# Optimization experiments

Measured on AMD Instinct MI355X. Metric: run time of the kernel, lower is better.

The kernel has to match this reference:

```python
import jax, jax.numpy as jnp
import numpy as np

B, T, C_IN, H, W = 64, 48, 64, 15, 15
HID, K, OUT = 128, 3, 128


def _conv(x, w, b):
    # x: [B, C, H, W], w: [4*HID, C, K, K] -> [B, 4*HID, H, W], SAME padding
    y = jax.lax.conv_general_dilated(
        x, w, window_strides=(1, 1), padding='SAME',
        dimension_numbers=('NCHW', 'OIHW', 'NCHW'))
    return y + b[None, :, None, None]


def _convlstm_layer(x_tm, w, b):
    # x_tm: time-major [T, B, C, H, W] -> hidden sequence [T, B, HID, H, W]
    h0 = jnp.zeros((x_tm.shape[1], HID, H, W), x_tm.dtype)
    c0 = jnp.zeros_like(h0)

    def step(carry, xt):
        h, c = carry
        z = _conv(jnp.concatenate([xt, h], axis=1), w, b)
        ig, fg, og, gg = jnp.split(z, 4, axis=1)
        i = jax.nn.sigmoid(ig)
        f = jax.nn.sigmoid(fg)
        o = jax.nn.sigmoid(og)
        g = jnp.tanh(gg)
        c_new = f * c + i * g
        h_new = o * jnp.tanh(c_new)
        return (h_new, c_new), h_new

    _, hs = jax.lax.scan(step, (h0, c0), x_tm)
    return hs


def setup_inputs() -> dict:
    key = jax.random.key(0)
    ks = jax.random.split(key, 7)
    s0 = 1.0 / np.sqrt((C_IN + HID) * K * K)
    s1 = 1.0 / np.sqrt((HID + HID) * K * K)
    sd = 1.0 / np.sqrt(HID * H * W)
    return {
        'encoder_output': jax.random.normal(ks[0], (B, T, C_IN, H, W), jnp.float32),
        'W0': jax.random.uniform(ks[1], (4 * HID, C_IN + HID, K, K), jnp.float32, -s0, s0),
        'b0': jax.random.uniform(ks[2], (4 * HID,), jnp.float32, -s0, s0),
        'W1': jax.random.uniform(ks[3], (4 * HID, HID + HID, K, K), jnp.float32, -s1, s1),
        'b1': jax.random.uniform(ks[4], (4 * HID,), jnp.float32, -s1, s1),
        'Wd': jax.random.uniform(ks[5], (HID * H * W, OUT), jnp.float32, -sd, sd),
        'bd': jax.random.uniform(ks[6], (OUT,), jnp.float32, -sd, sd),
    }


def reference(encoder_output, W0, b0, W1, b1, Wd, bd):
    x_tm = jnp.swapaxes(encoder_output, 0, 1)  # [T, B, C, H, W]
    h1 = _convlstm_layer(x_tm, W0, b0)          # [T, B, HID, H, W]
    h2 = _convlstm_layer(h1, W1, b1)            # [T, B, HID, H, W]
    last = h2[-1]                               # [B, HID, H, W] (last timestep)
    feat = last.reshape(last.shape[0], -1)      # dropout is identity in eval
    return feat @ Wd + bd
```

## Files before the change

kernel.cpp:

```cpp
#include <hip/hip_runtime.h>
#include <stdint.h>


typedef unsigned int u32;
typedef unsigned short u16;
typedef __attribute__((ext_vector_type(8))) short short8;
typedef __attribute__((ext_vector_type(4))) float f32x4;

#define NB    64
#define NT    48
#define NCX   64
#define NHID  128
#define NPIX  225
#define MTOT  (NB*NPIX)
#define MT_TILES 113
#define RROWS 18544
#define AROWS 224
#define L1BLK 216
#define L2BLK 288

__device__ __forceinline__ u32 bf16_rne(u32 u) {
  return (u + 0x7fffu + ((u >> 16) & 1u)) >> 16;
}
__device__ __forceinline__ float bf2f(u16 h) { return __uint_as_float(((u32)h) << 16); }
__device__ __forceinline__ void split2(float f, u32& hi, u32& lo) {
  u32 u = __float_as_uint(f);
  hi = bf16_rne(u);
  lo = bf16_rne(__float_as_uint(f - __uint_as_float(hi << 16)));
}
__device__ __forceinline__ void splitpair(u32 p0, u32 p1, u32& hw, u32& lw) {
  u32 s0, s1; u32 h0, l0, h1, l1;
  split2(__uint_as_float(p0), h0, l0);
  split2(__uint_as_float(p1), h1, l1);
  hw = (h1 << 16) | h0; lw = (l1 << 16) | l0;
  (void)s0; (void)s1;
}
__device__ __forceinline__ float sigmoidf_(float x) { return 1.f / (1.f + __expf(-x)); }
__device__ __forceinline__ float tanhf_(float x) {
  float e = __expf(-2.f * fabsf(x));
  return copysignf((1.f - e) / (1.f + e), x);
}
__device__ __forceinline__ void gl_lds16(const void* g, void* l) {
  __builtin_amdgcn_global_load_lds(
      (const __attribute__((address_space(1))) u32*)(g),
      (__attribute__((address_space(3))) u32*)(l), 16, 0, 0);
}

__global__ void prep_kernel(const float* __restrict__ W0, const float* __restrict__ b0,
                            const float* __restrict__ W1, const float* __restrict__ b1,
                            u16* __restrict__ Wi, float* __restrict__ bp) {
  const int total = (L1BLK + L2BLK) * 8192 + 1024;
  for (int idx = blockIdx.x * blockDim.x + threadIdx.x; idx < total;
       idx += gridDim.x * blockDim.x) {
    if (idx < (L1BLK + L2BLK) * 8192) {
      const int blk = idx >> 13, o = idx & 8191;
      int nt, cg, tap, CINL;
      const float* W;
      if (blk < L1BLK) { nt = blk / 54; cg = (blk % 54) / 9; tap = blk % 9; CINL = 192; W = W0; }
      else { const int b2 = blk - L1BLK; nt = b2 / 72; cg = (b2 % 72) / 9; tap = b2 % 9; CINL = 256; W = W1; }
      const int pl = o >> 12, kg = (o >> 10) & 3, qrow = (o >> 3) & 127, j = o & 7;
      const int q = nt * 128 + qrow;
      const int hid = ((q >> 6) << 4) | (q & 15), gate = (q >> 4) & 3;
      const int co = gate * 128 + hid;
      const int ci = cg * 32 + kg * 8 + j;
      const float wv = W[(size_t)co * (CINL * 9) + ci * 9 + tap];
      u32 hi, lo; split2(wv, hi, lo);
      Wi[idx] = (u16)(pl ? lo : hi);
    } else {
      const int e2 = idx - (L1BLK + L2BLK) * 8192;
      const int l = e2 >> 9, q = e2 & 511;
      const int hid = ((q >> 6) << 4) | (q & 15), gate = (q >> 4) & 3;
      bp[e2] = (l == 0 ? b0 : b1)[gate * 128 + hid];
    }
  }
}

template <int LAYER>
__device__ __forceinline__ void step_body(
    uint4* ldsA, uint4* ldsB, int mt, int nt,
    const float* __restrict__ x, int t,
    const u16* __restrict__ P1h, const u16* __restrict__ P1l,
    const u16* __restrict__ P2h, const u16* __restrict__ P2l,
    u16* __restrict__ Wh, u16* __restrict__ Wl,
    const u16* __restrict__ Wimg, const float* __restrict__ bp,
    float* __restrict__ c)
{
  constexpr int CG = (LAYER == 1) ? 6 : 8;
  const int tid = threadIdx.x, lane = tid & 63, w = tid >> 6;
  const int wave_m = (w >> 1) * 64, wave_n = (w & 1) * 64;
  const int kgc = lane >> 4, l15 = lane & 15;

  const int m0 = mt * 128;
  const int b0v = m0 / 225, p0v = m0 - b0v * 225;
  const int r0 = b0v * 289 + (p0v / 15) * 17 + (p0v % 15);

  int aoff[4];
  #pragma unroll
  for (int mb = 0; mb < 4; ++mb) {
    int m = m0 + wave_m + mb * 16 + l15; if (m > 14399) m = 14399;
    const int b = m / 225, p = m - b * 225;
    const int r = b * 289 + (p / 15) * 17 + (p % 15) + 18;
    aoff[mb] = (kgc * AROWS + (r - r0 - 18)) * 16;
  }
  int boff[4];
  #pragma unroll
  for (int nb = 0; nb < 4; ++nb) boff[nb] = (kgc * 128 + wave_n + l15 + nb * 16) * 16;

  f32x4 acc[4][4];
  #pragma unroll
  for (int i = 0; i < 4; ++i)
    #pragma unroll
    for (int j = 0; j < 4; ++j) acc[i][j] = (f32x4){0.f, 0.f, 0.f, 0.f};

  auto stageA_h = [&](const u16* __restrict__ Ph, const u16* __restrict__ Pl, int choff) {
    #pragma unroll
    for (int i = 0; i < 7; ++i) {
      const int chunk = w * 7 + i;
      const int e = chunk * 64 + lane;
      const int pk = e / AROWS, row = e - pk * AROWS;
      const int kg = pk & 3;
      const u16* P = (pk >= 4) ? Pl : Ph;
      const char* src = (const char*)P + ((size_t)(r0 + row) * 128 + choff + kg * 8) * 2;
      gl_lds16(src, (char*)ldsA + chunk * 1024);
    }
  };
  auto stageA_x = [&](int cg) {
    for (int tau = tid; tau < 4 * AROWS; tau += 256) {
      const int kg = tau / AROWS, row = tau - kg * AROWS;
      const int rg = r0 + row;
      const int rb = rg / 289, rr = rg - rb * 289;
      const int rh = rr / 17 - 1, rw = rr - (rr / 17) * 17 - 1;
      const bool v = ((unsigned)rh < 15u) && ((unsigned)rw < 15u) && (rb < 64);
      const int p = rh * 15 + rw;
      const float* src = x + (((size_t)rb * NT + t) * NCX + cg * 32 + kg * 8) * NPIX + p;
      u32 hw_[4], lw_[4];
      #pragma unroll
      for (int jj = 0; jj < 4; ++jj) {
        const float f0 = v ? src[(2 * jj) * NPIX] : 0.f;
        const float f1 = v ? src[(2 * jj + 1) * NPIX] : 0.f;
        u32 h0, l0, h1, l1;
        split2(f0, h0, l0); split2(f1, h1, l1);
        hw_[jj] = (h1 << 16) | h0; lw_[jj] = (l1 << 16) | l0;
      }
      ldsA[kg * AROWS + row]       = make_uint4(hw_[0], hw_[1], hw_[2], hw_[3]);
      ldsA[(4 + kg) * AROWS + row] = make_uint4(lw_[0], lw_[1], lw_[2], lw_[3]);
    }
  };
  auto stageB = [&](int cg, int tap, int bufsel) {
    const char* src = (const char*)Wimg + ((size_t)((nt * CG + cg) * 9 + tap) << 14);
    char* dstb = (char*)(ldsB + bufsel * 1024);
    #pragma unroll
    for (int j = 0; j < 4; ++j) {
      const int chunk = w * 4 + j;
      gl_lds16(src + chunk * 1024 + lane * 16, dstb + chunk * 1024);
    }
  };

  int bufsel = 0;
  for (int cg = 0; cg < CG; ++cg) {
    if (LAYER == 1 && cg < 2) stageA_x(cg);
    else if (LAYER == 1)      stageA_h(P1h, P1l, (cg - 2) * 32);
    else if (cg < 4)          stageA_h(P1h, P1l, cg * 32);
    else                      stageA_h(P2h, P2l, (cg - 4) * 32);
    if (cg == 0) stageB(0, 0, bufsel);
    __syncthreads();

    #pragma unroll
    for (int tap = 0; tap < 9; ++tap) {
      if (tap < 8)            stageB(cg, tap + 1, bufsel ^ 1);
      else if (cg + 1 < CG)   stageB(cg + 1, 0, bufsel ^ 1);
      {
        const int DPO = ((tap / 3) * 17 + (tap % 3)) * 16;
        const char* A  = (const char*)ldsA;
        const char* Bb = (const char*)(ldsB + bufsel * 1024);
        short8 ah[4], al[4], bh[4], bl[4];
        #pragma unroll
        for (int mb = 0; mb < 4; ++mb) {
          ah[mb] = *(const short8*)(A + aoff[mb] + DPO);
          al[mb] = *(const short8*)(A + aoff[mb] + DPO + 14336);
        }
        #pragma unroll
        for (int nb = 0; nb < 4; ++nb) {
          bh[nb] = *(const short8*)(Bb + boff[nb]);
          bl[nb] = *(const short8*)(Bb + boff[nb] + 8192);
        }
        __builtin_amdgcn_s_setprio(1);
        #pragma unroll
        for (int mb = 0; mb < 4; ++mb)
          #pragma unroll
          for (int nb = 0; nb < 4; ++nb) {
            acc[mb][nb] = __builtin_amdgcn_mfma_f32_16x16x32_bf16(ah[mb], bh[nb], acc[mb][nb], 0, 0, 0);
            acc[mb][nb] = __builtin_amdgcn_mfma_f32_16x16x32_bf16(al[mb], bh[nb], acc[mb][nb], 0, 0, 0);
            acc[mb][nb] = __builtin_amdgcn_mfma_f32_16x16x32_bf16(ah[mb], bl[nb], acc[mb][nb], 0, 0, 0);
          }
        __builtin_amdgcn_s_setprio(0);
      }
      __syncthreads();
      bufsel ^= 1;
    }
  }

  const int colq = nt * 128 + wave_n;
  const int hid  = ((colq >> 6) << 4) + l15;
  const float bi  = bp[colq +      l15];
  const float bf_ = bp[colq + 16 + l15];
  const float bo  = bp[colq + 32 + l15];
  const float bg  = bp[colq + 48 + l15];
  #pragma unroll
  for (int mb = 0; mb < 4; ++mb) {
    #pragma unroll
    for (int rr = 0; rr < 4; ++rr) {
      const int m = m0 + wave_m + mb * 16 + ((lane >> 4) << 2) + rr;
      if (m < MTOT) {
        const float gi = sigmoidf_(acc[mb][0][rr] + bi);
        const float gf = sigmoidf_(acc[mb][1][rr] + bf_);
        const float go = sigmoidf_(acc[mb][2][rr] + bo);
        const float gg = tanhf_   (acc[mb][3][rr] + bg);
        const size_t cidx = (size_t)m * NHID + hid;
        const float cn = gf * c[cidx] + gi * gg;
        c[cidx] = cn;
        const float h = go * tanhf_(cn);
        u32 hh, hl2; split2(h, hh, hl2);
        const int b = m / 225, p = m - b * 225;
        const size_t r = (size_t)b * 289 + (p / 15) * 17 + (p % 15) + 18;
        Wh[r * 128 + hid] = (u16)hh;
        Wl[r * 128 + hid] = (u16)hl2;
      }
    }
  }
}

__global__ __launch_bounds__(256, 2)
void steps_kernel(const float* __restrict__ x, int t1,
                  const u16* __restrict__ h1hr, const u16* __restrict__ h1lr,
                  const u16* __restrict__ h2hr, const u16* __restrict__ h2lr,
                  u16* __restrict__ h1hw, u16* __restrict__ h1lw,
                  u16* __restrict__ h2hw, u16* __restrict__ h2lw,
                  const u16* __restrict__ Wi, const float* __restrict__ bp,
                  float* __restrict__ c1, float* __restrict__ c2, int do_l2) {
  __shared__ uint4 ldsA[1792];
  __shared__ uint4 ldsB[2048];
  int bid = ((int)blockIdx.z * 4 + (int)blockIdx.y) * MT_TILES + (int)blockIdx.x;
  int nid = bid;
  if (gridDim.z == 2) nid = (bid & 7) * MT_TILES + (bid >> 3);
  const int z   = nid / (MT_TILES * 4);
  const int rem = nid - z * (MT_TILES * 4);
  const int nt  = rem / MT_TILES;
  const int mt  = rem - nt * MT_TILES;
  if (z == 0 && do_l2)
    step_body<2>(ldsA, ldsB, mt, nt, nullptr, 0, h1hr, h1lr, h2hr, h2lr,
                 h2hw, h2lw, Wi + (size_t)L1BLK * 8192, bp + 512, c2);
  else
    step_body<1>(ldsA, ldsB, mt, nt, x, t1, h1hr, h1lr, nullptr, nullptr,
                 h1hw, h1lw, Wi, bp, c1);
}

__global__ __launch_bounds__(256)
void dense_kernel(const u16* __restrict__ H2h, const u16* __restrict__ H2l,
                  const float* __restrict__ Wd, float* __restrict__ part) {
  __shared__ float sfeat[1800];
  __shared__ float red[128];
  const int b = blockIdx.x, ks = blockIdx.y, tid = threadIdx.x;
  for (int idx = tid; idx < 1800; idx += 256) {
    const int hid_l = idx & 7, pix = idx >> 3;
    const size_t r = (size_t)b * 289 + (pix / 15) * 17 + (pix % 15) + 18;
    const size_t si = r * 128 + ks * 8 + hid_l;
    sfeat[hid_l * 225 + pix] = bf2f(H2h[si]) + bf2f(H2l[si]);
  }
  __syncthreads();
  const int kk2 = tid >> 7, n = tid & 127;
  const float* wdp = Wd + (size_t)ks * 1800 * 128 + n;
  float s = 0.f;
  #pragma unroll 4
  for (int i = kk2; i < 1800; i += 2)
    s = fmaf(sfeat[i], wdp[(size_t)i * 128], s);
  if (kk2) red[n] = s;
  __syncthreads();
  if (!kk2) part[((size_t)b * 16 + ks) * 128 + n] = s + red[n];
}
__global__ void dense_reduce(const float* __restrict__ part, const float* __restrict__ bd,
                             float* __restrict__ out) {
  const int b = blockIdx.x, n = threadIdx.x;
  float s = bd[n];
  #pragma unroll
  for (int ks = 0; ks < 16; ++ks) s += part[((size_t)b * 16 + ks) * 128 + n];
  out[b * 128 + n] = s;
}

extern "C" void kernel_launch(void* const* d_in, const int* in_sizes, int n_in,
                              void* d_out, int out_size, void* d_ws, size_t ws_size,
                              hipStream_t stream) {
  const float* x  = (const float*)d_in[0];
  const float* W0 = (const float*)d_in[1];
  const float* b0 = (const float*)d_in[2];
  const float* W1 = (const float*)d_in[3];
  const float* b1 = (const float*)d_in[4];
  const float* Wd = (const float*)d_in[5];
  const float* bd = (const float*)d_in[6];

  const size_t HPB = (size_t)RROWS * 128 * 2;
  const size_t CSZ = (size_t)MTOT * NHID * 4;
  char* base = (char*)d_ws;
  u16* h1h[2] = { (u16*)(base),            (u16*)(base + HPB) };
  u16* h1l[2] = { (u16*)(base + 2 * HPB),  (u16*)(base + 3 * HPB) };
  u16* h2h[2] = { (u16*)(base + 4 * HPB),  (u16*)(base + 5 * HPB) };
  u16* h2l[2] = { (u16*)(base + 6 * HPB),  (u16*)(base + 7 * HPB) };
  float* c1 = (float*)(base + 8 * HPB);
  float* c2 = (float*)(base + 8 * HPB + CSZ);
  u16* Wi   = (u16*)(base + 8 * HPB + 2 * CSZ);
  const size_t WIB = (size_t)(L1BLK + L2BLK) * 16384;
  float* bp   = (float*)((char*)Wi + WIB);
  float* part = bp + 1024;
  const size_t need = 8 * HPB + 2 * CSZ + WIB + 1024 * 4 + (size_t)64 * 16 * 128 * 4;
  if (ws_size < need) return;

  hipMemsetAsync(d_ws, 0, 8 * HPB + 2 * CSZ, stream);
  prep_kernel<<<2048, 256, 0, stream>>>(W0, b0, W1, b1, Wi, bp);

  for (int k = -1; k <= 47; ++k) {
    const int rd = k & 1, wr = (k + 1) & 1;
    const int dl2 = (k >= 0), dl1 = (k <= 46);
    dim3 grid(MT_TILES, 4, dl1 + dl2);
    steps_kernel<<<grid, 256, 0, stream>>>(x, k + 1,
        h1h[rd], h1l[rd], h2h[rd], h2l[rd],
        h1h[wr], h1l[wr], h2h[wr], h2l[wr],
        Wi, bp, c1, c2, dl2);
  }
  dense_kernel<<<dim3(64, 16), 256, 0, stream>>>(h2h[0], h2l[0], Wd, part);
  dense_reduce<<<64, 128, 0, stream>>>(part, bd, (float*)d_out);
}
```

Measured before the change: 9.226 ms.

## Load weight fragments directly to registers and double-buffer A tile in LDS

```diff
diff --git a/kernel.cpp b/kernel.cpp
--- a/kernel.cpp
+++ b/kernel.cpp
@@ -14,7 +14,7 @@
 #define NPIX  225
 #define MTOT  (NB*NPIX)
 #define MT_TILES 113
-#define RROWS 18544
+#define RROWS 18624
 #define AROWS 224
 #define L1BLK 216
 #define L2BLK 288
@@ -27,13 +27,6 @@
   u32 u = __float_as_uint(f);
   hi = bf16_rne(u);
   lo = bf16_rne(__float_as_uint(f - __uint_as_float(hi << 16)));
-}
-__device__ __forceinline__ void splitpair(u32 p0, u32 p1, u32& hw, u32& lw) {
-  u32 s0, s1; u32 h0, l0, h1, l1;
-  split2(__uint_as_float(p0), h0, l0);
-  split2(__uint_as_float(p1), h1, l1);
-  hw = (h1 << 16) | h0; lw = (l1 << 16) | l0;
-  (void)s0; (void)s1;
 }
 __device__ __forceinline__ float sigmoidf_(float x) { return 1.f / (1.f + __expf(-x)); }
 __device__ __forceinline__ float tanhf_(float x) {
@@ -77,7 +70,7 @@
 
 template <int LAYER>
 __device__ __forceinline__ void step_body(
-    uint4* ldsA, uint4* ldsB, int mt, int nt,
+    uint4* ldsA, int mt, int nt,
     const float* __restrict__ x, int t,
     const u16* __restrict__ P1h, const u16* __restrict__ P1l,
     const u16* __restrict__ P2h, const u16* __restrict__ P2l,
@@ -102,9 +95,12 @@
     const int r = b * 289 + (p / 15) * 17 + (p % 15) + 18;
     aoff[mb] = (kgc * AROWS + (r - r0 - 18)) * 16;
   }
-  int boff[4];
-  #pragma unroll
-  for (int nb = 0; nb < 4; ++nb) boff[nb] = (kgc * 128 + wave_n + l15 + nb * 16) * 16;
+  int boffh[4], boffl[4];
+  #pragma unroll
+  for (int nb = 0; nb < 4; ++nb) {
+    boffh[nb] = (kgc * 128 + wave_n + l15 + nb * 16) * 16;
+    boffl[nb] = boffh[nb] + 8192;
+  }
 
   f32x4 acc[4][4];
   #pragma unroll
@@ -112,7 +108,8 @@
     #pragma unroll
     for (int j = 0; j < 4; ++j) acc[i][j] = (f32x4){0.f, 0.f, 0.f, 0.f};
 
-  auto stageA_h = [&](const u16* __restrict__ Ph, const u16* __restrict__ Pl, int choff) {
+  auto stageA_h = [&](const u16* __restrict__ Ph, const u16* __restrict__ Pl,
+                      int choff, uint4* dst) {
     #pragma unroll
     for (int i = 0; i < 7; ++i) {
       const int chunk = w * 7 + i;
@@ -121,10 +118,10 @@
       const int kg = pk & 3;
       const u16* P = (pk >= 4) ? Pl : Ph;
       const char* src = (const char*)P + ((size_t)(r0 + row) * 128 + choff + kg * 8) * 2;
-      gl_lds16(src, (char*)ldsA + chunk * 1024);
+      gl_lds16(src, (char*)dst + chunk * 1024);
     }
   };
-  auto stageA_x = [&](int cg) {
+  auto stageA_x = [&](int cg, uint4* dst) {
     for (int tau = tid; tau < 4 * AROWS; tau += 256) {
       const int kg = tau / AROWS, row = tau - kg * AROWS;
       const int rg = r0 + row;
@@ -142,62 +139,66 @@
         split2(f0, h0, l0); split2(f1, h1, l1);
         hw_[jj] = (h1 << 16) | h0; lw_[jj] = (l1 << 16) | l0;
       }
-      ldsA[kg * AROWS + row]       = make_uint4(hw_[0], hw_[1], hw_[2], hw_[3]);
-      ldsA[(4 + kg) * AROWS + row] = make_uint4(lw_[0], lw_[1], lw_[2], lw_[3]);
+      dst[kg * AROWS + row]       = make_uint4(hw_[0], hw_[1], hw_[2], hw_[3]);
+      dst[(4 + kg) * AROWS + row] = make_uint4(lw_[0], lw_[1], lw_[2], lw_[3]);
     }
   };
-  auto stageB = [&](int cg, int tap, int bufsel) {
-    const char* src = (const char*)Wimg + ((size_t)((nt * CG + cg) * 9 + tap) << 14);
-    char* dstb = (char*)(ldsB + bufsel * 1024);
-    #pragma unroll
-    for (int j = 0; j < 4; ++j) {
-      const int chunk = w * 4 + j;
-      gl_lds16(src + chunk * 1024 + lane * 16, dstb + chunk * 1024);
+  auto stageA = [&](int cg, uint4* dst) {
+    if (LAYER == 1) {
+      if (cg < 2) stageA_x(cg, dst);
+      else        stageA_h(P1h, P1l, (cg - 2) * 32, dst);
+    } else {
+      if (cg < 4) stageA_h(P1h, P1l, cg * 32, dst);
+      else        stageA_h(P2h, P2l, (cg - 4) * 32, dst);
     }
   };
 
-  int bufsel = 0;
+  stageA(0, ldsA);
+  __syncthreads();
   for (int cg = 0; cg < CG; ++cg) {
-    if (LAYER == 1 && cg < 2) stageA_x(cg);
-    else if (LAYER == 1)      stageA_h(P1h, P1l, (cg - 2) * 32);
-    else if (cg < 4)          stageA_h(P1h, P1l, cg * 32);
-    else                      stageA_h(P2h, P2l, (cg - 4) * 32);
-    if (cg == 0) stageB(0, 0, bufsel);
-    __syncthreads();
-
+    const uint4* cbuf = ldsA + (cg & 1) * 1792;
+    uint4* nbuf = ldsA + ((cg + 1) & 1) * 1792;
+    const char* wb = (const char*)Wimg + (((size_t)(nt * CG + cg) * 9) << 14);
+
+    short8 bh[2][4], bl[2][4];
+    #pragma unroll
+    for (int nb = 0; nb < 4; ++nb) {
+      bh[0][nb] = *(const short8*)(wb + boffh[nb]);
+      bl[0][nb] = *(const short8*)(wb + boffl[nb]);
+    }
     #pragma unroll
     for (int tap = 0; tap < 9; ++tap) {
-      if (tap < 8)            stageB(cg, tap + 1, bufsel ^ 1);
-      else if (cg + 1 < CG)   stageB(cg + 1, 0, bufsel ^ 1);
-      {
-        const int DPO = ((tap / 3) * 17 + (tap % 3)) * 16;
-        const char* A  = (const char*)ldsA;
-        const char* Bb = (const char*)(ldsB + bufsel * 1024);
-        short8 ah[4], al[4], bh[4], bl[4];
-        #pragma unroll
-        for (int mb = 0; mb < 4; ++mb) {
-          ah[mb] = *(const short8*)(A + aoff[mb] + DPO);
-          al[mb] = *(const short8*)(A + aoff[mb] + DPO + 14336);
-        }
+      const int cur = tap & 1, nxt = cur ^ 1;
+      if (tap < 8) {
+        const char* wbn = wb + ((size_t)(tap + 1) << 14);
         #pragma unroll
         for (int nb = 0; nb < 4; ++nb) {
-          bh[nb] = *(const short8*)(Bb + boff[nb]);
-          bl[nb] = *(const short8*)(Bb + boff[nb] + 8192);
+          bh[nxt][nb] = *(const short8*)(wbn + boffh[nb]);
+          bl[nxt][nb] = *(const short8*)(wbn + boffl[nb]);
         }
-        __builtin_amdgcn_s_setprio(1);
+      }
+      if (tap == 1 && cg + 1 < CG) stageA(cg + 1, nbuf);
+
+      const int DPO = ((tap / 3) * 17 + (tap % 3)) * 16;
+      const char* A = (const char*)cbuf;
+      short8 ah[4], al[4];
+      #pragma unroll
+      for (int mb = 0; mb < 4; ++mb) {
+        ah[mb] = *(const short8*)(A + aoff[mb] + DPO);
+        al[mb] = *(const short8*)(A + aoff[mb] + DPO + 14336);
+      }
+      __builtin_amdgcn_s_setprio(1);
+      #pragma unroll
+      for (int mb = 0; mb < 4; ++mb)
         #pragma unroll
-        for (int mb = 0; mb < 4; ++mb)
-          #pragma unroll
-          for (int nb = 0; nb < 4; ++nb) {
-            acc[mb][nb] = __builtin_amdgcn_mfma_f32_16x16x32_bf16(ah[mb], bh[nb], acc[mb][nb], 0, 0, 0);
-            acc[mb][nb] = __builtin_amdgcn_mfma_f32_16x16x32_bf16(al[mb], bh[nb], acc[mb][nb], 0, 0, 0);
-            acc[mb][nb] = __builtin_amdgcn_mfma_f32_16x16x32_bf16(ah[mb], bl[nb], acc[mb][nb], 0, 0, 0);
-          }
-        __builtin_amdgcn_s_setprio(0);
-      }
-      __syncthreads();
-      bufsel ^= 1;
-    }
+        for (int nb = 0; nb < 4; ++nb) {
+          acc[mb][nb] = __builtin_amdgcn_mfma_f32_16x16x32_bf16(ah[mb], bh[cur][nb], acc[mb][nb], 0, 0, 0);
+          acc[mb][nb] = __builtin_amdgcn_mfma_f32_16x16x32_bf16(al[mb], bh[cur][nb], acc[mb][nb], 0, 0, 0);
+          acc[mb][nb] = __builtin_amdgcn_mfma_f32_16x16x32_bf16(ah[mb], bl[cur][nb], acc[mb][nb], 0, 0, 0);
+        }
+      __builtin_amdgcn_s_setprio(0);
+    }
+    __syncthreads();
   }
 
   const int colq = nt * 128 + wave_n;
@@ -238,8 +239,7 @@
                   u16* __restrict__ h2hw, u16* __restrict__ h2lw,
                   const u16* __restrict__ Wi, const float* __restrict__ bp,
                   float* __restrict__ c1, float* __restrict__ c2, int do_l2) {
-  __shared__ uint4 ldsA[1792];
-  __shared__ uint4 ldsB[2048];
+  __shared__ uint4 ldsA[3584];
   int bid = ((int)blockIdx.z * 4 + (int)blockIdx.y) * MT_TILES + (int)blockIdx.x;
   int nid = bid;
   if (gridDim.z == 2) nid = (bid & 7) * MT_TILES + (bid >> 3);
@@ -248,10 +248,10 @@
   const int nt  = rem / MT_TILES;
   const int mt  = rem - nt * MT_TILES;
   if (z == 0 && do_l2)
-    step_body<2>(ldsA, ldsB, mt, nt, nullptr, 0, h1hr, h1lr, h2hr, h2lr,
+    step_body<2>(ldsA, mt, nt, nullptr, 0, h1hr, h1lr, h2hr, h2lr,
                  h2hw, h2lw, Wi + (size_t)L1BLK * 8192, bp + 512, c2);
   else
-    step_body<1>(ldsA, ldsB, mt, nt, x, t1, h1hr, h1lr, nullptr, nullptr,
+    step_body<1>(ldsA, mt, nt, x, t1, h1hr, h1lr, nullptr, nullptr,
                  h1hw, h1lw, Wi, bp, c1);
 }
 
```

Result: faster. 8.447 ms (-8.4%).
